# Kernel optimization log

Measured on AMD Instinct MI355X. Metric: run time of the kernel, lower is better.

## Reference

```python
import jax, jax.numpy as jnp
import numpy as np

NEG_INF = -1000000.0  # matches torch masked_fill constant


def setup_inputs() -> dict:
    key = jax.random.key(0)
    k1, k2, k3, k4 = jax.random.split(key, 4)
    B, Lq, Lk, d = 64, 1024, 1024, 64
    queries = jax.random.normal(k1, (B, Lq, d), dtype=jnp.float32)
    keys = jax.random.normal(k2, (B, Lk, d), dtype=jnp.float32)
    values = jax.random.normal(k3, (B, Lk, d), dtype=jnp.float32)
    valid_lens = jax.random.randint(k4, (B,), 0, 1024, dtype=jnp.int64)
    return {"queries": queries, "keys": keys, "values": values, "valid_lens": valid_lens}


def reference(queries, keys, values, valid_lens):
    d = queries.shape[-1]
    # [B, Lq, Lk] scores
    scores = jnp.einsum("bqd,bkd->bqk", queries, keys) / jnp.sqrt(jnp.float32(d))
    Lk = scores.shape[-1]
    # valid_lens is per-batch (dim 1 in torch): same mask across all query rows
    mask = jnp.arange(Lk)[None, None, :] < valid_lens[:, None, None]  # [B,1,Lk]
    scores = jnp.where(mask, scores, NEG_INF)
    attn = jax.nn.softmax(scores, axis=-1)
    # dropout p=0.0 -> identity
    return jnp.einsum("bqk,bkd->bqd", attn, values)
```

## Files before the change

### kernel.cpp

```cpp
#include <hip/hip_runtime.h>
#include <hip/hip_bf16.h>

#define NEG_BIG -1000000.0f

typedef __attribute__((ext_vector_type(8))) short short8;
typedef __attribute__((ext_vector_type(4))) short short4v;
typedef __attribute__((ext_vector_type(4))) float floatx4;

#if __has_builtin(__builtin_amdgcn_exp2f)
#define EXP2F(x) __builtin_amdgcn_exp2f(x)
#else
#define EXP2F(x) exp2f(x)
#endif

#if __has_builtin(__builtin_amdgcn_mfma_f32_16x16x16bf16_1k)
#define MFMA16(a, b, c) __builtin_amdgcn_mfma_f32_16x16x16bf16_1k(a, b, c, 0, 0, 0)
#else
static __device__ __forceinline__ floatx4 MFMA16_fn(short4v a, short4v b, floatx4 c) {
    floatx4 d;
    asm("v_mfma_f32_16x16x16_bf16 %0, %1, %2, %3\n\ts_nop 4"
        : "=v"(d) : "v"(a), "v"(b), "v"(c));
    return d;
}
#define MFMA16(a, b, c) MFMA16_fn(a, b, c)
#endif

static __device__ __forceinline__ unsigned short bf16u(float f) {
    union { __hip_bfloat16 h; unsigned short u; } c;
    c.h = __float2bfloat16(f);
    return c.u;
}

static __device__ __forceinline__ short8 pack8(float4 a, float4 b) {
    union { short8 s; __hip_bfloat162 h[4]; } u;
    u.h[0] = __float22bfloat162_rn(make_float2(a.x, a.y));
    u.h[1] = __float22bfloat162_rn(make_float2(a.z, a.w));
    u.h[2] = __float22bfloat162_rn(make_float2(b.x, b.y));
    u.h[3] = __float22bfloat162_rn(make_float2(b.z, b.w));
    return u.s;
}

__global__ __launch_bounds__(256, 3)
void attn_fwd(const float* __restrict__ Q, const float* __restrict__ K,
              const float* __restrict__ V, const int* __restrict__ vlen,
              float* __restrict__ out)
{
    __shared__ __attribute__((aligned(16))) unsigned short K_lds[2][4096];
    __shared__ __attribute__((aligned(16))) unsigned short VT_lds[2][4096];

    const int bid  = blockIdx.x;
    const int orig = (bid & 7) * 128 + (bid >> 3);
    const int b    = orig >> 4;
    const int qc   = orig & 15;

    const int tid = threadIdx.x;
    const int l   = tid & 63;
    const int w   = tid >> 6;
    const int lr  = l & 15;
    const int lg  = l >> 4;

    const float* Qb = Q + (size_t)b * 65536;
    const float* Kb = K + (size_t)b * 65536;
    const float* Vb = V + (size_t)b * 65536;

    const int valid = vlen[b];
    const int kmax  = (valid == 0) ? 1024 : valid;
    const int ntile = (kmax + 63) >> 6;

    const float qscale = 0.18033688011112042f;
    short8 qf[2];
#pragma unroll
    for (int c = 0; c < 2; ++c) {
        const float* p = Qb + (size_t)(qc*64 + w*16 + lr) * 64 + c*32 + lg*8;
        float4 a = *(const float4*)p, bb = *(const float4*)(p + 4);
        a.x *= qscale; a.y *= qscale; a.z *= qscale; a.w *= qscale;
        bb.x *= qscale; bb.y *= qscale; bb.z *= qscale; bb.w *= qscale;
        qf[c] = pack8(a, bb);
    }

    floatx4 o[4];
#pragma unroll
    for (int n = 0; n < 4; ++n) o[n] = (floatx4){0.f, 0.f, 0.f, 0.f};
    float m = -INFINITY, lsum = 0.f;

    const int row   = w * 16 + (l >> 2);
    const int cbase = (l & 3) * 16;

    float4 kra[4], vra[4];

#define LOAD_K(T) do {                                                      \
    const float* pk = Kb + (size_t)((T)*64 + row) * 64 + cbase;             \
    kra[0] = *(const float4*)pk;       kra[1] = *(const float4*)(pk + 4);   \
    kra[2] = *(const float4*)(pk + 8); kra[3] = *(const float4*)(pk + 12);  \
    } while (0)

#define LOAD_V(T) do {                                                      \
    const float* pv = Vb + (size_t)((T)*64 + row) * 64 + cbase;             \
    vra[0] = *(const float4*)pv;       vra[1] = *(const float4*)(pv + 4);   \
    vra[2] = *(const float4*)(pv + 8); vra[3] = *(const float4*)(pv + 12);  \
    } while (0)

#define WRITE_K(B) do {                                                     \
    const int _fk = (row & 7) * 8;                                          \
    *(short8*)&K_lds[B][row*64 + (cbase ^ _fk)]       = pack8(kra[0], kra[1]); \
    *(short8*)&K_lds[B][row*64 + ((cbase + 8) ^ _fk)] = pack8(kra[2], kra[3]); \
    } while (0)

#define WRITE_V(B) do {                                                     \
    _Pragma("unroll")                                                       \
    for (int j = 0; j < 16; ++j) {                                          \
        const int dv = cbase + j;                                           \
        const int fv = ((dv & 7) ^ (dv >> 3)) * 8;                          \
        VT_lds[B][dv*64 + (row ^ fv)] = bf16u(((const float*)&vra[j>>2])[j&3]); \
    } } while (0)

    LOAD_K(0);
    LOAD_V(0);
    WRITE_K(0);
    WRITE_V(0);
    __syncthreads();

    for (int t = 0; t < ntile; ++t) {
        const int cur = t & 1;
        const int nxt = cur ^ 1;
        const int k0  = t * 64;
        const bool pf = (t + 1 < ntile);

        if (pf) { LOAD_K(t + 1); LOAD_V(t + 1); }

        floatx4 sa[4];
        __builtin_amdgcn_s_setprio(1);
#pragma unroll
        for (int n = 0; n < 4; ++n) {
            const int kr = n*16 + lr;
            const int fk = (lr & 7) * 8;
            const short8 kf0 = *(const short8*)&K_lds[cur][kr*64 + ((lg*8)      ^ fk)];
            const short8 kf1 = *(const short8*)&K_lds[cur][kr*64 + ((32 + lg*8) ^ fk)];
            sa[n] = (floatx4){0.f, 0.f, 0.f, 0.f};
            sa[n] = __builtin_amdgcn_mfma_f32_16x16x32_bf16(kf0, qf[0], sa[n], 0, 0, 0);
            sa[n] = __builtin_amdgcn_mfma_f32_16x16x32_bf16(kf1, qf[1], sa[n], 0, 0, 0);
        }
        __builtin_amdgcn_s_setprio(0);

        if ((k0 + 64) > valid) {
            const int kb = k0 + lg*4;
#pragma unroll
            for (int n = 0; n < 4; ++n)
#pragma unroll
            for (int r = 0; r < 4; ++r)
                sa[n][r] = (kb + n*16 + r >= valid) ? NEG_BIG : sa[n][r];
        }

        float rmax = fmaxf(
            fmaxf(fmaxf(fmaxf(sa[0][0], sa[0][1]), fmaxf(sa[0][2], sa[0][3])),
                  fmaxf(fmaxf(sa[1][0], sa[1][1]), fmaxf(sa[1][2], sa[1][3]))),
            fmaxf(fmaxf(fmaxf(sa[2][0], sa[2][1]), fmaxf(sa[2][2], sa[2][3])),
                  fmaxf(fmaxf(sa[3][0], sa[3][1]), fmaxf(sa[3][2], sa[3][3]))));
        rmax = fmaxf(rmax, __shfl_xor(rmax, 16));
        rmax = fmaxf(rmax, __shfl_xor(rmax, 32));

        const float nm = fmaxf(m, rmax);
        const float sc = EXP2F(m - nm);
        m = nm;

        float rs = 0.f;
#pragma unroll
        for (int n = 0; n < 4; ++n)
#pragma unroll
        for (int r = 0; r < 4; ++r) {
            sa[n][r] = EXP2F(sa[n][r] - m);
            rs += sa[n][r];
        }
        rs += __shfl_xor(rs, 16);
        rs += __shfl_xor(rs, 32);
        lsum = lsum * sc + rs;

        float sc_r[4];
#pragma unroll
        for (int r = 0; r < 4; ++r) sc_r[r] = __shfl(sc, lg*4 + r);
#pragma unroll
        for (int n = 0; n < 4; ++n)
#pragma unroll
        for (int r = 0; r < 4; ++r) o[n][r] *= sc_r[r];

        short4v pk[4];
#pragma unroll
        for (int n = 0; n < 4; ++n) {
            union { short4v s; __hip_bfloat162 h[2]; } u;
            u.h[0] = __float22bfloat162_rn(make_float2(sa[n][0], sa[n][1]));
            u.h[1] = __float22bfloat162_rn(make_float2(sa[n][2], sa[n][3]));
            pk[n] = u.s;
        }

        if (pf) WRITE_K(nxt);

        __builtin_amdgcn_s_setprio(1);
#pragma unroll
        for (int kc = 0; kc < 4; ++kc) {
#pragma unroll
            for (int n2 = 0; n2 < 4; ++n2) {
                const int dv = n2*16 + lr;
                const int fv = ((dv & 7) ^ (dv >> 3)) * 8;
                const short4v vf = *(const short4v*)&VT_lds[cur][dv*64 + ((kc*16 + lg*4) ^ fv)];
                o[n2] = MFMA16(pk[kc], vf, o[n2]);
            }
        }
        __builtin_amdgcn_s_setprio(0);

        if (pf) WRITE_V(nxt);
        __syncthreads();
    }

    const float inv = 1.0f / lsum;
    float inv_r[4];
#pragma unroll
    for (int r = 0; r < 4; ++r) inv_r[r] = __shfl(inv, lg*4 + r);

    float* Ob = out + (size_t)b * 65536;
#pragma unroll
    for (int n = 0; n < 4; ++n)
#pragma unroll
    for (int r = 0; r < 4; ++r) {
        const int q = qc*64 + w*16 + lg*4 + r;
        Ob[(size_t)q * 64 + n*16 + lr] = o[n][r] * inv_r[r];
    }
#undef LOAD_K
#undef LOAD_V
#undef WRITE_K
#undef WRITE_V
}

extern "C" void kernel_launch(void* const* d_in, const int* in_sizes, int n_in,
                              void* d_out, int out_size, void* d_ws, size_t ws_size,
                              hipStream_t stream) {
    (void)in_sizes; (void)n_in; (void)d_ws; (void)ws_size; (void)out_size;
    const float* Q  = (const float*)d_in[0];
    const float* K  = (const float*)d_in[1];
    const float* V  = (const float*)d_in[2];
    const int*   vl = (const int*)d_in[3];
    float* O = (float*)d_out;
    attn_fwd<<<dim3(1024), dim3(256), 0, stream>>>(Q, K, V, vl, O);
}
```

Before: 45.29 us.

## Split KV range into two chunks with merge kernel, lazy rescale, permlane reductions

Splits each (batch, query-chunk) work item across two KV halves, launching 2048 blocks that write partial outputs plus row max and sum to workspace, then a merge kernel combines them. This aims to balance load across batches whose valid lengths vary. It also skips the running-max rescale when the new max stays within a threshold, and uses permlane swap builtins for the cross-lane reductions. The costs are a second launch and extra workspace traffic. The split path only runs if the workspace is large enough, which is not known.

```diff
diff --git a/kernel.cpp b/kernel.cpp
--- a/kernel.cpp
+++ b/kernel.cpp
@@ -25,6 +25,30 @@
 #define MFMA16(a, b, c) MFMA16_fn(a, b, c)
 #endif
 
+#if __has_builtin(__builtin_amdgcn_permlane16_swap) && __has_builtin(__builtin_amdgcn_permlane32_swap)
+static __device__ __forceinline__ float redmax16_32(float x) {
+    auto a = __builtin_amdgcn_permlane16_swap(__float_as_int(x), __float_as_int(x), false, false);
+    x = fmaxf(__int_as_float(a[0]), __int_as_float(a[1]));
+    auto b = __builtin_amdgcn_permlane32_swap(__float_as_int(x), __float_as_int(x), false, false);
+    return fmaxf(__int_as_float(b[0]), __int_as_float(b[1]));
+}
+static __device__ __forceinline__ float redsum16_32(float x) {
+    auto a = __builtin_amdgcn_permlane16_swap(__float_as_int(x), __float_as_int(x), false, false);
+    x = __int_as_float(a[0]) + __int_as_float(a[1]);
+    auto b = __builtin_amdgcn_permlane32_swap(__float_as_int(x), __float_as_int(x), false, false);
+    return __int_as_float(b[0]) + __int_as_float(b[1]);
+}
+#else
+static __device__ __forceinline__ float redmax16_32(float x) {
+    x = fmaxf(x, __shfl_xor(x, 16));
+    return fmaxf(x, __shfl_xor(x, 32));
+}
+static __device__ __forceinline__ float redsum16_32(float x) {
+    x += __shfl_xor(x, 16);
+    return x + __shfl_xor(x, 32);
+}
+#endif
+
 static __device__ __forceinline__ unsigned short bf16u(float f) {
     union { __hip_bfloat16 h; unsigned short u; } c;
     c.h = __float2bfloat16(f);
@@ -40,18 +64,31 @@
     return u.s;
 }
 
+template<bool SPLIT>
 __global__ __launch_bounds__(256, 3)
 void attn_fwd(const float* __restrict__ Q, const float* __restrict__ K,
               const float* __restrict__ V, const int* __restrict__ vlen,
-              float* __restrict__ out)
+              float* __restrict__ out, float* __restrict__ ws)
 {
     __shared__ __attribute__((aligned(16))) unsigned short K_lds[2][4096];
     __shared__ __attribute__((aligned(16))) unsigned short VT_lds[2][4096];
 
-    const int bid  = blockIdx.x;
-    const int orig = (bid & 7) * 128 + (bid >> 3);
-    const int b    = orig >> 4;
-    const int qc   = orig & 15;
+    const int bid = blockIdx.x;
+    int b, qc, chunk;
+    if (SPLIT) {
+        const int orig = (bid & 7) * 256 + (bid >> 3);
+        b = orig >> 5; chunk = (orig >> 4) & 1; qc = orig & 15;
+    } else {
+        const int orig = (bid & 7) * 128 + (bid >> 3);
+        b = orig >> 4; chunk = 0; qc = orig & 15;
+    }
+
+    const int valid = vlen[b];
+    const int kmax  = (valid == 0) ? 1024 : valid;
+    const int ntile = (kmax + 63) >> 6;
+    const int tstart = SPLIT ? chunk * 8 : 0;
+    const int tend   = SPLIT ? min(ntile, tstart + 8) : ntile;
+    if (SPLIT && tstart >= tend) return;
 
     const int tid = threadIdx.x;
     const int l   = tid & 63;
@@ -62,10 +99,6 @@
     const float* Qb = Q + (size_t)b * 65536;
     const float* Kb = K + (size_t)b * 65536;
     const float* Vb = V + (size_t)b * 65536;
-
-    const int valid = vlen[b];
-    const int kmax  = (valid == 0) ? 1024 : valid;
-    const int ntile = (kmax + 63) >> 6;
 
     const float qscale = 0.18033688011112042f;
     short8 qf[2];
@@ -114,17 +147,17 @@
         VT_lds[B][dv*64 + (row ^ fv)] = bf16u(((const float*)&vra[j>>2])[j&3]); \
     } } while (0)
 
-    LOAD_K(0);
-    LOAD_V(0);
+    LOAD_K(tstart);
+    LOAD_V(tstart);
     WRITE_K(0);
     WRITE_V(0);
     __syncthreads();
 
-    for (int t = 0; t < ntile; ++t) {
-        const int cur = t & 1;
+    for (int t = tstart; t < tend; ++t) {
+        const int cur = (t - tstart) & 1;
         const int nxt = cur ^ 1;
         const int k0  = t * 64;
-        const bool pf = (t + 1 < ntile);
+        const bool pf = (t + 1 < tend);
 
         if (pf) { LOAD_K(t + 1); LOAD_V(t + 1); }
 
@@ -156,12 +189,21 @@
                   fmaxf(fmaxf(sa[1][0], sa[1][1]), fmaxf(sa[1][2], sa[1][3]))),
             fmaxf(fmaxf(fmaxf(sa[2][0], sa[2][1]), fmaxf(sa[2][2], sa[2][3])),
                   fmaxf(fmaxf(sa[3][0], sa[3][1]), fmaxf(sa[3][2], sa[3][3]))));
-        rmax = fmaxf(rmax, __shfl_xor(rmax, 16));
-        rmax = fmaxf(rmax, __shfl_xor(rmax, 32));
-
-        const float nm = fmaxf(m, rmax);
-        const float sc = EXP2F(m - nm);
-        m = nm;
+        rmax = redmax16_32(rmax);
+
+        if (!__all(rmax <= m + 11.0f)) {
+            const float nm = fmaxf(m, rmax);
+            const float sc = EXP2F(m - nm);
+            m = nm;
+            lsum *= sc;
+            float sc_r[4];
+#pragma unroll
+            for (int r = 0; r < 4; ++r) sc_r[r] = __shfl(sc, lg*4 + r);
+#pragma unroll
+            for (int n = 0; n < 4; ++n)
+#pragma unroll
+            for (int r = 0; r < 4; ++r) o[n][r] *= sc_r[r];
+        }
 
         float rs = 0.f;
 #pragma unroll
@@ -171,17 +213,7 @@
             sa[n][r] = EXP2F(sa[n][r] - m);
             rs += sa[n][r];
         }
-        rs += __shfl_xor(rs, 16);
-        rs += __shfl_xor(rs, 32);
-        lsum = lsum * sc + rs;
-
-        float sc_r[4];
-#pragma unroll
-        for (int r = 0; r < 4; ++r) sc_r[r] = __shfl(sc, lg*4 + r);
-#pragma unroll
-        for (int n = 0; n < 4; ++n)
-#pragma unroll
-        for (int r = 0; r < 4; ++r) o[n][r] *= sc_r[r];
+        lsum += redsum16_32(rs);
 
         short4v pk[4];
 #pragma unroll
@@ -211,18 +243,38 @@
         __syncthreads();
     }
 
-    const float inv = 1.0f / lsum;
-    float inv_r[4];
-#pragma unroll
-    for (int r = 0; r < 4; ++r) inv_r[r] = __shfl(inv, lg*4 + r);
-
-    float* Ob = out + (size_t)b * 65536;
-#pragma unroll
-    for (int n = 0; n < 4; ++n)
-#pragma unroll
-    for (int r = 0; r < 4; ++r) {
-        const int q = qc*64 + w*16 + lg*4 + r;
-        Ob[(size_t)q * 64 + n*16 + lr] = o[n][r] * inv_r[r];
+    if (!SPLIT || ntile <= 8) {
+        const float inv = 1.0f / lsum;
+        float inv_r[4];
+#pragma unroll
+        for (int r = 0; r < 4; ++r) inv_r[r] = __shfl(inv, lg*4 + r);
+        float* Ob = out + (size_t)b * 65536;
+#pragma unroll
+        for (int n = 0; n < 4; ++n)
+#pragma unroll
+        for (int r = 0; r < 4; ++r) {
+            const int q = qc*64 + w*16 + lg*4 + r;
+            Ob[(size_t)q * 64 + n*16 + lr] = o[n][r] * inv_r[r];
+        }
+    } else {
+        float* wsb = ws + ((size_t)((b*16 + qc)*2 + chunk)) * 4224;
+        float m_r[4], l_r[4];
+#pragma unroll
+        for (int r = 0; r < 4; ++r) {
+            m_r[r] = __shfl(m,    lg*4 + r);
+            l_r[r] = __shfl(lsum, lg*4 + r);
+        }
+#pragma unroll
+        for (int n = 0; n < 4; ++n)
+#pragma unroll
+        for (int r = 0; r < 4; ++r) {
+            const int q_loc = w*16 + lg*4 + r;
+            wsb[q_loc*64 + n*16 + lr] = o[n][r];
+        }
+        if (lg == 0) {
+            wsb[4096 + w*16 + lr] = m;
+            wsb[4160 + w*16 + lr] = lsum;
+        }
     }
 #undef LOAD_K
 #undef LOAD_V
@@ -230,14 +282,60 @@
 #undef WRITE_V
 }
 
+__global__ __launch_bounds__(256)
+void attn_merge(const int* __restrict__ vlen, const float* __restrict__ ws,
+                float* __restrict__ out)
+{
+    const int site = blockIdx.x;
+    const int b    = site >> 4;
+    const int qc   = site & 15;
+    const int valid = vlen[b];
+    const int kmax  = (valid == 0) ? 1024 : valid;
+    if (kmax <= 512) return;
+
+    const int tid   = threadIdx.x;
+    const int q_loc = tid >> 2;
+    const int dg    = (tid & 3) * 16;
+
+    const float* w0 = ws + (size_t)site * 2 * 4224;
+    const float* w1 = w0 + 4224;
+    const float m0 = w0[4096 + q_loc], l0 = w0[4160 + q_loc];
+    const float m1 = w1[4096 + q_loc], l1 = w1[4160 + q_loc];
+    const float M  = fmaxf(m0, m1);
+    const float a0 = EXP2F(m0 - M), a1 = EXP2F(m1 - M);
+    const float inv = 1.0f / (l0 * a0 + l1 * a1);
+
+    const float4* o0 = (const float4*)(w0 + q_loc*64 + dg);
+    const float4* o1 = (const float4*)(w1 + q_loc*64 + dg);
+    float4* dst = (float4*)(out + ((size_t)(b*1024 + qc*64 + q_loc)) * 64 + dg);
+#pragma unroll
+    for (int i = 0; i < 4; ++i) {
+        const float4 p = o0[i], q = o1[i];
+        float4 r;
+        r.x = (p.x * a0 + q.x * a1) * inv;
+        r.y = (p.y * a0 + q.y * a1) * inv;
+        r.z = (p.z * a0 + q.z * a1) * inv;
+        r.w = (p.w * a0 + q.w * a1) * inv;
+        dst[i] = r;
+    }
+}
+
 extern "C" void kernel_launch(void* const* d_in, const int* in_sizes, int n_in,
                               void* d_out, int out_size, void* d_ws, size_t ws_size,
                               hipStream_t stream) {
-    (void)in_sizes; (void)n_in; (void)d_ws; (void)ws_size; (void)out_size;
+    (void)in_sizes; (void)n_in; (void)out_size;
     const float* Q  = (const float*)d_in[0];
     const float* K  = (const float*)d_in[1];
     const float* V  = (const float*)d_in[2];
     const int*   vl = (const int*)d_in[3];
-    float* O = (float*)d_out;
-    attn_fwd<<<dim3(1024), dim3(256), 0, stream>>>(Q, K, V, vl, O);
-}
+    float* O  = (float*)d_out;
+    float* WS = (float*)d_ws;
+
+    const size_t need = (size_t)1024 * 2 * 4224 * sizeof(float);
+    if (ws_size >= need) {
+        attn_fwd<true><<<dim3(2048), dim3(256), 0, stream>>>(Q, K, V, vl, O, WS);
+        attn_merge<<<dim3(1024), dim3(256), 0, stream>>>(vl, WS, O);
+    } else {
+        attn_fwd<false><<<dim3(1024), dim3(256), 0, stream>>>(Q, K, V, vl, O, WS);
+    }
+}
```

Result: slower. 52.98 us (+17.0%).

## Use persistent blocks with an atomic work queue and lazy softmax rescaling

Applied to the files above, without the earlier changes.

Launches a fixed grid of 768 persistent blocks that take (batch, query-chunk) work items from a global atomic counter, which is zeroed in the workspace before each launch. The aim is to balance load across CUs, since tile counts vary with the per-batch valid length. The online softmax now skips the running max update and the output rescale unless the new row max exceeds the old one by more than 11 in the log2 domain. Cross-lane max and sum reductions use permlane16/32 swaps instead of shuffles. The trade-offs are an extra memset, a per-item atomic plus barrier, and loss of the previous XCD-aware block-to-batch swizzle.

```diff
diff --git a/kernel.cpp b/kernel.cpp
--- a/kernel.cpp
+++ b/kernel.cpp
@@ -25,6 +25,30 @@
 #define MFMA16(a, b, c) MFMA16_fn(a, b, c)
 #endif
 
+#if __has_builtin(__builtin_amdgcn_permlane16_swap) && __has_builtin(__builtin_amdgcn_permlane32_swap)
+static __device__ __forceinline__ float redmax16_32(float x) {
+    auto a = __builtin_amdgcn_permlane16_swap(__float_as_int(x), __float_as_int(x), false, false);
+    x = fmaxf(__int_as_float(a[0]), __int_as_float(a[1]));
+    auto b = __builtin_amdgcn_permlane32_swap(__float_as_int(x), __float_as_int(x), false, false);
+    return fmaxf(__int_as_float(b[0]), __int_as_float(b[1]));
+}
+static __device__ __forceinline__ float redsum16_32(float x) {
+    auto a = __builtin_amdgcn_permlane16_swap(__float_as_int(x), __float_as_int(x), false, false);
+    x = __int_as_float(a[0]) + __int_as_float(a[1]);
+    auto b = __builtin_amdgcn_permlane32_swap(__float_as_int(x), __float_as_int(x), false, false);
+    return __int_as_float(b[0]) + __int_as_float(b[1]);
+}
+#else
+static __device__ __forceinline__ float redmax16_32(float x) {
+    x = fmaxf(x, __shfl_xor(x, 16));
+    return fmaxf(x, __shfl_xor(x, 32));
+}
+static __device__ __forceinline__ float redsum16_32(float x) {
+    x += __shfl_xor(x, 16);
+    return x + __shfl_xor(x, 32);
+}
+#endif
+
 static __device__ __forceinline__ unsigned short bf16u(float f) {
     union { __hip_bfloat16 h; unsigned short u; } c;
     c.h = __float2bfloat16(f);
@@ -43,15 +67,11 @@
 __global__ __launch_bounds__(256, 3)
 void attn_fwd(const float* __restrict__ Q, const float* __restrict__ K,
               const float* __restrict__ V, const int* __restrict__ vlen,
-              float* __restrict__ out)
+              float* __restrict__ out, int* __restrict__ ctr)
 {
     __shared__ __attribute__((aligned(16))) unsigned short K_lds[2][4096];
     __shared__ __attribute__((aligned(16))) unsigned short VT_lds[2][4096];
-
-    const int bid  = blockIdx.x;
-    const int orig = (bid & 7) * 128 + (bid >> 3);
-    const int b    = orig >> 4;
-    const int qc   = orig & 15;
+    __shared__ int s_site;
 
     const int tid = threadIdx.x;
     const int l   = tid & 63;
@@ -59,34 +79,28 @@
     const int lr  = l & 15;
     const int lg  = l >> 4;
 
-    const float* Qb = Q + (size_t)b * 65536;
-    const float* Kb = K + (size_t)b * 65536;
-    const float* Vb = V + (size_t)b * 65536;
-
-    const int valid = vlen[b];
-    const int kmax  = (valid == 0) ? 1024 : valid;
-    const int ntile = (kmax + 63) >> 6;
-
-    const float qscale = 0.18033688011112042f;
-    short8 qf[2];
-#pragma unroll
-    for (int c = 0; c < 2; ++c) {
-        const float* p = Qb + (size_t)(qc*64 + w*16 + lr) * 64 + c*32 + lg*8;
-        float4 a = *(const float4*)p, bb = *(const float4*)(p + 4);
-        a.x *= qscale; a.y *= qscale; a.z *= qscale; a.w *= qscale;
-        bb.x *= qscale; bb.y *= qscale; bb.z *= qscale; bb.w *= qscale;
-        qf[c] = pack8(a, bb);
-    }
-
-    floatx4 o[4];
-#pragma unroll
-    for (int n = 0; n < 4; ++n) o[n] = (floatx4){0.f, 0.f, 0.f, 0.f};
-    float m = -INFINITY, lsum = 0.f;
-
     const int row   = w * 16 + (l >> 2);
     const int cbase = (l & 3) * 16;
 
-    float4 kra[4], vra[4];
+    const float qscale = 0.18033688011112042f;
+
+    for (;;) {
+        if (tid == 0) s_site = atomicAdd(ctr, 1);
+        __syncthreads();
+        const int site = s_site;
+        if (site >= 1024) return;
+        const int b  = site >> 4;
+        const int qc = site & 15;
+
+        const int valid = vlen[b];
+        const int kmax  = (valid == 0) ? 1024 : valid;
+        const int ntile = (kmax + 63) >> 6;
+
+        const float* Qb = Q + (size_t)b * 65536;
+        const float* Kb = K + (size_t)b * 65536;
+        const float* Vb = V + (size_t)b * 65536;
+
+        float4 kra[4], vra[4];
 
 #define LOAD_K(T) do {                                                      \
     const float* pk = Kb + (size_t)((T)*64 + row) * 64 + cbase;             \
@@ -114,130 +128,150 @@
         VT_lds[B][dv*64 + (row ^ fv)] = bf16u(((const float*)&vra[j>>2])[j&3]); \
     } } while (0)
 
-    LOAD_K(0);
-    LOAD_V(0);
-    WRITE_K(0);
-    WRITE_V(0);
-    __syncthreads();
-
-    for (int t = 0; t < ntile; ++t) {
-        const int cur = t & 1;
-        const int nxt = cur ^ 1;
-        const int k0  = t * 64;
-        const bool pf = (t + 1 < ntile);
-
-        if (pf) { LOAD_K(t + 1); LOAD_V(t + 1); }
-
-        floatx4 sa[4];
-        __builtin_amdgcn_s_setprio(1);
-#pragma unroll
-        for (int n = 0; n < 4; ++n) {
-            const int kr = n*16 + lr;
-            const int fk = (lr & 7) * 8;
-            const short8 kf0 = *(const short8*)&K_lds[cur][kr*64 + ((lg*8)      ^ fk)];
-            const short8 kf1 = *(const short8*)&K_lds[cur][kr*64 + ((32 + lg*8) ^ fk)];
-            sa[n] = (floatx4){0.f, 0.f, 0.f, 0.f};
-            sa[n] = __builtin_amdgcn_mfma_f32_16x16x32_bf16(kf0, qf[0], sa[n], 0, 0, 0);
-            sa[n] = __builtin_amdgcn_mfma_f32_16x16x32_bf16(kf1, qf[1], sa[n], 0, 0, 0);
+        LOAD_K(0);
+        LOAD_V(0);
+
+        short8 qf[2];
+#pragma unroll
+        for (int c = 0; c < 2; ++c) {
+            const float* p = Qb + (size_t)(qc*64 + w*16 + lr) * 64 + c*32 + lg*8;
+            float4 a = *(const float4*)p, bb = *(const float4*)(p + 4);
+            a.x *= qscale; a.y *= qscale; a.z *= qscale; a.w *= qscale;
+            bb.x *= qscale; bb.y *= qscale; bb.z *= qscale; bb.w *= qscale;
+            qf[c] = pack8(a, bb);
         }
-        __builtin_amdgcn_s_setprio(0);
-
-        if ((k0 + 64) > valid) {
-            const int kb = k0 + lg*4;
+
+        floatx4 o[4];
+#pragma unroll
+        for (int n = 0; n < 4; ++n) o[n] = (floatx4){0.f, 0.f, 0.f, 0.f};
+        float m = -INFINITY, lsum = 0.f;
+
+        WRITE_K(0);
+        WRITE_V(0);
+        __syncthreads();
+
+        for (int t = 0; t < ntile; ++t) {
+            const int cur = t & 1;
+            const int nxt = cur ^ 1;
+            const int k0  = t * 64;
+            const bool pf = (t + 1 < ntile);
+
+            if (pf) { LOAD_K(t + 1); LOAD_V(t + 1); }
+
+            floatx4 sa[4];
+            __builtin_amdgcn_s_setprio(1);
+#pragma unroll
+            for (int n = 0; n < 4; ++n) {
+                const int kr = n*16 + lr;
+                const int fk = (lr & 7) * 8;
+                const short8 kf0 = *(const short8*)&K_lds[cur][kr*64 + ((lg*8)      ^ fk)];
+                const short8 kf1 = *(const short8*)&K_lds[cur][kr*64 + ((32 + lg*8) ^ fk)];
+                sa[n] = (floatx4){0.f, 0.f, 0.f, 0.f};
+                sa[n] = __builtin_amdgcn_mfma_f32_16x16x32_bf16(kf0, qf[0], sa[n], 0, 0, 0);
+                sa[n] = __builtin_amdgcn_mfma_f32_16x16x32_bf16(kf1, qf[1], sa[n], 0, 0, 0);
+            }
+            __builtin_amdgcn_s_setprio(0);
+
+            if ((k0 + 64) > valid) {
+                const int kb = k0 + lg*4;
+#pragma unroll
+                for (int n = 0; n < 4; ++n)
+#pragma unroll
+                for (int r = 0; r < 4; ++r)
+                    sa[n][r] = (kb + n*16 + r >= valid) ? NEG_BIG : sa[n][r];
+            }
+
+            float rmax = fmaxf(
+                fmaxf(fmaxf(fmaxf(sa[0][0], sa[0][1]), fmaxf(sa[0][2], sa[0][3])),
+                      fmaxf(fmaxf(sa[1][0], sa[1][1]), fmaxf(sa[1][2], sa[1][3]))),
+                fmaxf(fmaxf(fmaxf(sa[2][0], sa[2][1]), fmaxf(sa[2][2], sa[2][3])),
+                      fmaxf(fmaxf(sa[3][0], sa[3][1]), fmaxf(sa[3][2], sa[3][3]))));
+            rmax = redmax16_32(rmax);
+
+            if (!__all(rmax <= m + 11.0f)) {
+                const float nm = fmaxf(m, rmax);
+                const float sc = EXP2F(m - nm);
+                m = nm;
+                lsum *= sc;
+                float sc_r[4];
+#pragma unroll
+                for (int r = 0; r < 4; ++r) sc_r[r] = __shfl(sc, lg*4 + r);
+#pragma unroll
+                for (int n = 0; n < 4; ++n)
+#pragma unroll
+                for (int r = 0; r < 4; ++r) o[n][r] *= sc_r[r];
+            }
+
+            float rs = 0.f;
 #pragma unroll
             for (int n = 0; n < 4; ++n)
 #pragma unroll
-            for (int r = 0; r < 4; ++r)
-                sa[n][r] = (kb + n*16 + r >= valid) ? NEG_BIG : sa[n][r];
+            for (int r = 0; r < 4; ++r) {
+                sa[n][r] = EXP2F(sa[n][r] - m);
+                rs += sa[n][r];
+            }
+            lsum += redsum16_32(rs);
+
+            short4v pk[4];
+#pragma unroll
+            for (int n = 0; n < 4; ++n) {
+                union { short4v s; __hip_bfloat162 h[2]; } u;
+                u.h[0] = __float22bfloat162_rn(make_float2(sa[n][0], sa[n][1]));
+                u.h[1] = __float22bfloat162_rn(make_float2(sa[n][2], sa[n][3]));
+                pk[n] = u.s;
+            }
+
+            if (pf) WRITE_K(nxt);
+
+            __builtin_amdgcn_s_setprio(1);
+#pragma unroll
+            for (int kc = 0; kc < 4; ++kc) {
+#pragma unroll
+                for (int n2 = 0; n2 < 4; ++n2) {
+                    const int dv = n2*16 + lr;
+                    const int fv = ((dv & 7) ^ (dv >> 3)) * 8;
+                    const short4v vf = *(const short4v*)&VT_lds[cur][dv*64 + ((kc*16 + lg*4) ^ fv)];
+                    o[n2] = MFMA16(pk[kc], vf, o[n2]);
+                }
+            }
+            __builtin_amdgcn_s_setprio(0);
+
+            if (pf) WRITE_V(nxt);
+            __syncthreads();
         }
 
-        float rmax = fmaxf(
-            fmaxf(fmaxf(fmaxf(sa[0][0], sa[0][1]), fmaxf(sa[0][2], sa[0][3])),
-                  fmaxf(fmaxf(sa[1][0], sa[1][1]), fmaxf(sa[1][2], sa[1][3]))),
-            fmaxf(fmaxf(fmaxf(sa[2][0], sa[2][1]), fmaxf(sa[2][2], sa[2][3])),
-                  fmaxf(fmaxf(sa[3][0], sa[3][1]), fmaxf(sa[3][2], sa[3][3]))));
-        rmax = fmaxf(rmax, __shfl_xor(rmax, 16));
-        rmax = fmaxf(rmax, __shfl_xor(rmax, 32));
-
-        const float nm = fmaxf(m, rmax);
-        const float sc = EXP2F(m - nm);
-        m = nm;
-
-        float rs = 0.f;
-#pragma unroll
-        for (int n = 0; n < 4; ++n)
-#pragma unroll
-        for (int r = 0; r < 4; ++r) {
-            sa[n][r] = EXP2F(sa[n][r] - m);
-            rs += sa[n][r];
+        {
+            const float inv = 1.0f / lsum;
+            float inv_r[4];
+#pragma unroll
+            for (int r = 0; r < 4; ++r) inv_r[r] = __shfl(inv, lg*4 + r);
+            float* Ob = out + (size_t)b * 65536;
+#pragma unroll
+            for (int n = 0; n < 4; ++n)
+#pragma unroll
+            for (int r = 0; r < 4; ++r) {
+                const int q = qc*64 + w*16 + lg*4 + r;
+                Ob[(size_t)q * 64 + n*16 + lr] = o[n][r] * inv_r[r];
+            }
         }
-        rs += __shfl_xor(rs, 16);
-        rs += __shfl_xor(rs, 32);
-        lsum = lsum * sc + rs;
-
-        float sc_r[4];
-#pragma unroll
-        for (int r = 0; r < 4; ++r) sc_r[r] = __shfl(sc, lg*4 + r);
-#pragma unroll
-        for (int n = 0; n < 4; ++n)
-#pragma unroll
-        for (int r = 0; r < 4; ++r) o[n][r] *= sc_r[r];
-
-        short4v pk[4];
-#pragma unroll
-        for (int n = 0; n < 4; ++n) {
-            union { short4v s; __hip_bfloat162 h[2]; } u;
-            u.h[0] = __float22bfloat162_rn(make_float2(sa[n][0], sa[n][1]));
-            u.h[1] = __float22bfloat162_rn(make_float2(sa[n][2], sa[n][3]));
-            pk[n] = u.s;
-        }
-
-        if (pf) WRITE_K(nxt);
-
-        __builtin_amdgcn_s_setprio(1);
-#pragma unroll
-        for (int kc = 0; kc < 4; ++kc) {
-#pragma unroll
-            for (int n2 = 0; n2 < 4; ++n2) {
-                const int dv = n2*16 + lr;
-                const int fv = ((dv & 7) ^ (dv >> 3)) * 8;
-                const short4v vf = *(const short4v*)&VT_lds[cur][dv*64 + ((kc*16 + lg*4) ^ fv)];
-                o[n2] = MFMA16(pk[kc], vf, o[n2]);
-            }
-        }
-        __builtin_amdgcn_s_setprio(0);
-
-        if (pf) WRITE_V(nxt);
-        __syncthreads();
-    }
-
-    const float inv = 1.0f / lsum;
-    float inv_r[4];
-#pragma unroll
-    for (int r = 0; r < 4; ++r) inv_r[r] = __shfl(inv, lg*4 + r);
-
-    float* Ob = out + (size_t)b * 65536;
-#pragma unroll
-    for (int n = 0; n < 4; ++n)
-#pragma unroll
-    for (int r = 0; r < 4; ++r) {
-        const int q = qc*64 + w*16 + lg*4 + r;
-        Ob[(size_t)q * 64 + n*16 + lr] = o[n][r] * inv_r[r];
-    }
 #undef LOAD_K
 #undef LOAD_V
 #undef WRITE_K
 #undef WRITE_V
+    }
 }
 
 extern "C" void kernel_launch(void* const* d_in, const int* in_sizes, int n_in,
                               void* d_out, int out_size, void* d_ws, size_t ws_size,
                               hipStream_t stream) {
-    (void)in_sizes; (void)n_in; (void)d_ws; (void)ws_size; (void)out_size;
+    (void)in_sizes; (void)n_in; (void)out_size; (void)ws_size;
     const float* Q  = (const float*)d_in[0];
     const float* K  = (const float*)d_in[1];
     const float* V  = (const float*)d_in[2];
     const int*   vl = (const int*)d_in[3];
-    float* O = (float*)d_out;
-    attn_fwd<<<dim3(1024), dim3(256), 0, stream>>>(Q, K, V, vl, O);
-}
+    float* O   = (float*)d_out;
+    int*   ctr = (int*)d_ws;
+
+    hipMemsetAsync(ctr, 0, sizeof(int), stream);
+    attn_fwd<<<dim3(768), dim3(256), 0, stream>>>(Q, K, V, vl, O, ctr);
+}
```

Result: slower. 54.16 us (+19.6%).
